# Optimization experiments

Hardware: AMD Instinct MI355X
Metric: run time of the kernel (lower is better)

The kernel has to match this reference:

```python
import jax, jax.numpy as jnp
import numpy as np
from jax import lax

RATE = 2
KSIZE = 3
STRIDE = 1
FUSE_K = 3
SCALE = 10.0
DN = ('NCHW', 'OIHW', 'NCHW')


def extract_patches(x, k, s):
    # x: [B,C,H,W] -> [B,nH,nW,C,k,k]  (ZeroPad2d(1) when k != 1, as in torch code)
    B, C, H, W = x.shape
    p = 0 if k == 1 else 1
    xp = jnp.pad(x, ((0, 0), (0, 0), (p, p), (p, p)))
    nH = (H + 2 * p - k) // s + 1
    nW = (W + 2 * p - k) // s + 1
    cols = [xp[:, :, di:di + s * nH:s, dj:dj + s * nW:s]
            for di in range(k) for dj in range(k)]
    pat = jnp.stack(cols, 0).reshape(k, k, B, C, nH, nW)
    return pat.transpose(2, 4, 5, 3, 0, 1)


def _fuse(y):
    # conv of the [L,L] score image with eye(FUSE_K) kernel, same padding
    # == sum of diagonal shifts of the zero-padded image
    L = y.shape[0]
    p = (FUSE_K - 1) // 2
    A = jnp.pad(y, ((p, p), (p, p)))
    out = A[0:L, 0:L]
    for d in range(1, FUSE_K):
        out = out + A[d:d + L, d:d + L]
    return out


def _per_sample(xi, wi, raw_wi, mmi, h, w):
    # xi: [C,h,w]  wi: [L,C,3,3]  raw_wi: [L,C,4,4]  mmi: [L,1,1]
    L = h * w
    norm = jnp.sqrt(jnp.sum(wi * wi, axis=(1, 2, 3), keepdims=True))
    wi_n = wi / jnp.maximum(norm, 1e-4)
    # cosine-similarity conv: [L,h,w]
    yi = lax.conv_general_dilated(xi[None], wi_n, (1, 1), ((1, 1), (1, 1)),
                                  dimension_numbers=DN)[0]
    # fuse pass 1 on [L(patch), L(spatial)]
    y = _fuse(yi.reshape(L, L))
    # transpose (h_p,w_p,h',w') -> (w_p,h_p,w',h'), fuse pass 2, transpose back
    y = y.reshape(h, w, h, w).transpose(1, 0, 3, 2).reshape(L, L)
    y = _fuse(y)
    y = y.reshape(w, h, w, h).transpose(1, 0, 3, 2).reshape(L, h, w)
    y = y * mmi
    y = jax.nn.softmax(y * SCALE, axis=0)
    y = jnp.maximum(y * mmi, 1e-8)
    # conv_transpose2d(y, raw_wi, stride=2, padding=1) as lhs-dilated conv
    Wf = raw_wi[:, :, ::-1, ::-1].transpose(1, 0, 2, 3)  # [C,L,4,4]
    out = lax.conv_general_dilated(y[None], Wf, (1, 1), ((2, 2), (2, 2)),
                                   lhs_dilation=(2, 2),
                                   dimension_numbers=DN)[0]
    return out / 4.0


def reference(x1, x2, mask):
    B, C, H, W = x1.shape
    kernel = 2 * RATE
    raw_w = extract_patches(x1, kernel, RATE * STRIDE)
    x2s = x2[:, :, ::2, ::2]          # F.interpolate scale=0.5, nearest
    h, w = x2s.shape[2], x2s.shape[3]
    L = h * w
    raw_w = raw_w.reshape(B, L, C, kernel, kernel)
    wpat = extract_patches(x2s, KSIZE, STRIDE).reshape(B, L, C, KSIZE, KSIZE)
    # mask is already [B,1,h,w]: bilinear align_corners resize to (h,w) is identity
    m = extract_patches(mask, KSIZE, STRIDE).reshape(B, L, -1).mean(axis=2)
    mm = (m == 0.0).astype(x1.dtype)[:, :, None, None]  # [B,L,1,1]
    f = lambda xi, wi, rwi, mmi: _per_sample(xi, wi, rwi, mmi, h, w)
    return jax.vmap(f)(x2s, wpat, raw_w, mm)  # [B,C,H,W]


def setup_inputs() -> dict:
    key = jax.random.key(0)
    k1, k2 = jax.random.split(key)
    x1 = jax.random.normal(k1, (2, 128, 96, 96), dtype=jnp.float32)
    x2 = jax.random.normal(k2, (2, 128, 96, 96), dtype=jnp.float32)
    mask = jnp.zeros((2, 1, 48, 48), dtype=jnp.float32)
    return {"x1": x1, "x2": x2, "mask": mask}
```

## Files before the change

kernel.cpp:

```cpp
#include <hip/hip_runtime.h>
#include <hip/hip_bf16.h>

#define Cc   128
#define Hh   96
#define hs   48
#define Ls   2304
#define CK   2048
#define KG   384

typedef __attribute__((ext_vector_type(8))) short short8;
typedef __attribute__((ext_vector_type(4))) float f32x4;

__device__ __forceinline__ unsigned short f2bf(float x) {
    unsigned int u = __float_as_uint(x);
    unsigned int r = (u + 0x7fff + ((u >> 16) & 1)) >> 16;
    return (unsigned short)r;
}
__device__ __forceinline__ float bf2f(unsigned short h) {
    return __uint_as_float((unsigned)h << 16);
}

__device__ __forceinline__ f32x4 ld4u(const float* p) {
    f32x4 v; __builtin_memcpy(&v, p, 16); return v;
}

#define GLOAD_LDS16(g, l) \
    __builtin_amdgcn_global_load_lds((__attribute__((address_space(1))) const void*)(g), \
                                     (__attribute__((address_space(3))) void*)(l), 16, 0, 0)


__global__ __launch_bounds__(256) void transposePQ_k(const float* __restrict__ x2,
                                                     unsigned short* __restrict__ P,
                                                     unsigned short* __restrict__ Q,
                                                     long long sPQ, int z0) {
    const int z = z0 + blockIdx.z;
    const float* x2b = x2 + (size_t)z * Cc * Hh * Hh;
    unsigned short* Pb = P + (size_t)blockIdx.z * sPQ;
    unsigned short* Qb = Q + (size_t)blockIdx.z * sPQ;
    __shared__ float tile[64][65];
    const int c0 = blockIdx.x * 64;
    const int l0 = blockIdx.y * 64;
    const int t = threadIdx.x;
    const int lt = t & 63, cg = t >> 6;
    const int l = l0 + lt;
    const int iy = l / hs, jx = l % hs;
    const int srcoff = iy * (2 * Hh) + 2 * jx;
#pragma unroll
    for (int cc = 0; cc < 16; ++cc) {
        int c = cg * 16 + cc;
        tile[lt][c] = x2b[(size_t)(c0 + c) * (Hh * Hh) + srcoff];
    }
    __syncthreads();
    const int lr = t >> 2, seg = t & 3;
    const int lw = l0 + lr;
    short8 hv0, hv1, lv0, lv1;
#pragma unroll
    for (int k = 0; k < 8; ++k) {
        float x = tile[lr][seg * 16 + k];
        unsigned short h = f2bf(x);
        float hf = __uint_as_float((unsigned)h << 16);
        unsigned short lo = f2bf(x - hf);
        hv0[k] = (short)h; lv0[k] = (short)lo;
    }
#pragma unroll
    for (int k = 0; k < 8; ++k) {
        float x = tile[lr][seg * 16 + 8 + k];
        unsigned short h = f2bf(x);
        float hf = __uint_as_float((unsigned)h << 16);
        unsigned short lo = f2bf(x - hf);
        hv1[k] = (short)h; lv1[k] = (short)lo;
    }
    size_t rowp = (size_t)lw * KG;
    int coff = c0 + seg * 16;
    *(short8*)&Pb[rowp + coff] = hv0;        *(short8*)&Pb[rowp + coff + 8] = hv1;
    *(short8*)&Pb[rowp + 128 + coff] = lv0;  *(short8*)&Pb[rowp + 128 + coff + 8] = lv1;
    *(short8*)&Pb[rowp + 256 + coff] = hv0;  *(short8*)&Pb[rowp + 256 + coff + 8] = hv1;
    *(short8*)&Qb[rowp + coff] = hv0;        *(short8*)&Qb[rowp + coff + 8] = hv1;
    *(short8*)&Qb[rowp + 128 + coff] = hv0;  *(short8*)&Qb[rowp + 128 + coff + 8] = hv1;
    *(short8*)&Qb[rowp + 256 + coff] = lv0;  *(short8*)&Qb[rowp + 256 + coff + 8] = lv1;
}

__global__ __launch_bounds__(256) void mm_k(const float* __restrict__ mask, float* __restrict__ MM) {
    int z = blockIdx.y;
    const float* mb = mask + (size_t)z * hs * hs;
    float* MMb = MM + (size_t)z * Ls;
    int l = blockIdx.x * 256 + threadIdx.x;
    if (l >= Ls) return;
    int ly = l / hs, lx = l % hs;
    float s = 0.f;
    for (int dy = -1; dy <= 1; ++dy)
        for (int dx = -1; dx <= 1; ++dx) {
            int yy = ly + dy, xx = lx + dx;
            if ((unsigned)yy < (unsigned)hs && (unsigned)xx < (unsigned)hs) s += mb[yy * hs + xx];
        }
    float m = s * (1.0f / 9.0f);
    MMb[l] = (m == 0.0f) ? 1.0f : 0.0f;
}

__global__ __launch_bounds__(256) void taps9rn_k(const float* __restrict__ G, float* __restrict__ S,
                                                 float* __restrict__ RN, long long zsG, long long zsS, int z0) {
    const float* Gb = G + (size_t)blockIdx.z * zsG;
    float* Sb = S + (size_t)blockIdx.z * zsS;
    float* RNb = RN + (size_t)(z0 + blockIdx.z) * Ls;
    int g = blockIdx.x * 256 + threadIdx.x;
    int i = g / 576;
    int jb = (g - i * 576) * 4;
    int iy = i / hs, ix = i % hs;
    int jy = jb / hs, jx0 = jb % hs;
    f32x4 acc = {};
#pragma unroll
    for (int dy = -1; dy <= 1; ++dy) {
        int vy = ((unsigned)(iy + dy) < (unsigned)hs) && ((unsigned)(jy + dy) < (unsigned)hs);
#pragma unroll
        for (int dx = -1; dx <= 1; ++dx) {
            int vi = vy && ((unsigned)(ix + dx) < (unsigned)hs);
            int o = hs * dy + dx;
            int row = vi ? (i + o) : i;
            f32x4 v = ld4u(&Gb[(size_t)row * Ls + jb + o]);
            f32x4 m;
#pragma unroll
            for (int ln = 0; ln < 4; ++ln)
                m[ln] = (vi && ((unsigned)(jx0 + ln + dx) < (unsigned)hs)) ? 1.f : 0.f;
            acc += v * m;
        }
    }
    __builtin_memcpy(&Sb[(size_t)i * Ls + jb], &acc, 16);
    int dd = i - jb;
    if ((unsigned)dd < 4u) RNb[i] = 1.0f / fmaxf(sqrtf(acc[dd]), 1e-4f);
}

__global__ __launch_bounds__(256) void fuse12T_k(const float* __restrict__ S, const float* __restrict__ RN,
                                                 float* __restrict__ ZT, long long zsS, long long zsZT, int z0) {
    const float* Sb = S + (size_t)blockIdx.z * zsS;
    float* ZTb = ZT + (size_t)blockIdx.z * zsZT;
    const float* RNb = RN + (size_t)(z0 + blockIdx.z) * Ls;
    __shared__ float tile[64][65];
    const int i0 = blockIdx.y * 64, j0 = blockIdx.x * 64;
    const int t = threadIdx.x;
    const int jg = t & 15, tit = t >> 4;
    const int jb = j0 + jg * 4;
    const int jy0 = jb / hs, jx0 = jb % hs;

    int ccb[9]; f32x4 m4[9];
#pragma unroll
    for (int d2 = -1; d2 <= 1; ++d2) {
        int cl[4], vb[4];
#pragma unroll
        for (int ln = 0; ln < 4; ++ln) {
            int j2 = (jx0 + ln) * hs + jy0 + d2;
            int vv = ((unsigned)j2 < (unsigned)Ls) ? 1 : 0;
            int c = vv ? ((j2 % hs) * hs + j2 / hs) : 0;
            cl[ln] = c; vb[ln] = vv;
        }
        int base = 0;
#pragma unroll
        for (int ln = 0; ln < 4; ++ln) if (vb[ln]) base = cl[ln] - ln;
#pragma unroll
        for (int d1 = -1; d1 <= 1; ++d1) {
            int idx = (d2 + 1) * 3 + (d1 + 1);
            ccb[idx] = base + d1;
            f32x4 mm;
#pragma unroll
            for (int ln = 0; ln < 4; ++ln) {
                int cc = cl[ln] + d1;
                mm[ln] = (vb[ln] && ((unsigned)cc < (unsigned)Ls)) ? 1.f : 0.f;
            }
            m4[idx] = mm;
        }
    }

    f32x4 acc[4] = {};
#pragma unroll
    for (int kk = 0; kk < 4; ++kk) {
        const int i = i0 + tit * 4 + kk;
        const int iy = i / hs, ix = i % hs;
        const int tif = ix * hs + iy;
#pragma unroll
        for (int d2 = -1; d2 <= 1; ++d2) {
            int i2 = tif + d2;
            int vi = ((unsigned)i2 < (unsigned)Ls) ? 1 : 0;
            int r = vi ? ((i2 % hs) * hs + i2 / hs) : 1;
#pragma unroll
            for (int d1 = -1; d1 <= 1; ++d1) {
                int rr = r + d1;
                int vr = vi && ((unsigned)rr < (unsigned)Ls);
                int rrc = vr ? rr : 0;
                float w = RNb[rrc];
                w = vr ? w : 0.f;
                int idx = (d2 + 1) * 3 + (d1 + 1);
                f32x4 v = ld4u(&Sb[(size_t)rrc * Ls + ccb[idx]]);
                acc[kk] += v * m4[idx] * w;
            }
        }
    }
#pragma unroll
    for (int kk = 0; kk < 4; ++kk) {
        int ti = tit * 4 + kk;
        tile[ti][jg * 4 + 0] = acc[kk][0];
        tile[ti][jg * 4 + 1] = acc[kk][1];
        tile[ti][jg * 4 + 2] = acc[kk][2];
        tile[ti][jg * 4 + 3] = acc[kk][3];
    }
    __syncthreads();
    const int r2 = t >> 2, cs = (t & 3) * 16;
    float vbuf[16];
#pragma unroll
    for (int k = 0; k < 16; ++k) vbuf[k] = tile[cs + k][r2];
    float* dst = &ZTb[(size_t)(j0 + r2) * Ls + i0 + cs];
#pragma unroll
    for (int k = 0; k < 4; ++k)
        *(float4*)&dst[k * 4] = *(float4*)&vbuf[k * 4];
}

__global__ __launch_bounds__(256) void softmax_row_k(const float* __restrict__ ZT, const float* __restrict__ MM,
                                                     unsigned short* __restrict__ AT, long long zsZT, int z0) {
    const int z = z0 + blockIdx.z;
    const float* ZTb = ZT + (size_t)blockIdx.z * zsZT;
    const float* MMb = MM + (size_t)z * Ls;
    unsigned short* ATb = AT + (size_t)z * Ls * Ls;
    const int w = threadIdx.x >> 6, lane = threadIdx.x & 63;
    const int p = blockIdx.x * 4 + w;
    const float* row = ZTb + (size_t)p * Ls;
    float v[36];
    float mx = -3.4e38f;
#pragma unroll
    for (int k = 0; k < 9; ++k) {
        const float4 zv = *(const float4*)&row[k * 256 + lane * 4];
        const float4 m = *(const float4*)&MMb[k * 256 + lane * 4];
        v[4 * k + 0] = zv.x * m.x * 10.f;
        v[4 * k + 1] = zv.y * m.y * 10.f;
        v[4 * k + 2] = zv.z * m.z * 10.f;
        v[4 * k + 3] = zv.w * m.w * 10.f;
        mx = fmaxf(mx, fmaxf(fmaxf(v[4 * k], v[4 * k + 1]), fmaxf(v[4 * k + 2], v[4 * k + 3])));
    }
#pragma unroll
    for (int off = 32; off; off >>= 1) mx = fmaxf(mx, __shfl_xor(mx, off));
    float sum = 0.f;
#pragma unroll
    for (int kk = 0; kk < 36; ++kk) { v[kk] = expf(v[kk] - mx); sum += v[kk]; }
#pragma unroll
    for (int off = 32; off; off >>= 1) sum += __shfl_xor(sum, off);
    const float rs = 1.0f / sum;
#pragma unroll
    for (int k = 0; k < 9; ++k) {
        const float4 m = *(const float4*)&MMb[k * 256 + lane * 4];
        ushort4 o;
        o.x = f2bf(fmaxf(v[4 * k + 0] * rs * m.x, 1e-8f));
        o.y = f2bf(fmaxf(v[4 * k + 1] * rs * m.y, 1e-8f));
        o.z = f2bf(fmaxf(v[4 * k + 2] * rs * m.z, 1e-8f));
        o.w = f2bf(fmaxf(v[4 * k + 3] * rs * m.w, 1e-8f));
        *(ushort4*)&ATb[(size_t)p * Ls + k * 256 + lane * 4] = o;
    }
}

__global__ __launch_bounds__(256) void gather_rwT_k(const float* __restrict__ x1, unsigned short* __restrict__ RWT) {
    const int z = blockIdx.z;
    const float* x1b = x1 + (size_t)z * Cc * Hh * Hh;
    unsigned short* R = RWT + (size_t)z * CK * Ls;
    int l = blockIdx.x * 256 + threadIdx.x;
    int ck = blockIdx.y;
    int c = ck >> 4, a = (ck >> 2) & 3, b2 = ck & 3;
    int ly = l / hs, lx = l % hs;
    int u = 2 * ly + a - 1, vv = 2 * lx + b2 - 1;
    float val = ((unsigned)u < (unsigned)Hh && (unsigned)vv < (unsigned)Hh) ? x1b[c * (Hh * Hh) + u * Hh + vv] : 0.0f;
    R[(size_t)ck * Ls + l] = f2bf(val);
}

__global__ __launch_bounds__(256) void scatter3_k(const unsigned short* __restrict__ T, float* __restrict__ out) {
    const int z = blockIdx.z;
    const int c = blockIdx.x;
    const int yh = blockIdx.y;
    const unsigned short* Tb = T + (size_t)z * Ls * CK + (size_t)c * 16;
    float* outb = out + (size_t)z * Cc * Hh * Hh + (size_t)c * Hh * Hh;
    const int i0 = (yh == 0) ? 0 : 23;
    __shared__ unsigned short Tl[1200 * 16];
    const int t = threadIdx.x;
#pragma unroll
    for (int rep = 0; rep < 5; ++rep) {
        int p = rep * 256 + t;
        if (p < 1200)
            __builtin_memcpy(&Tl[p * 16], &Tb[(size_t)(i0 * hs + p) * CK], 32);
    }
    __syncthreads();
#pragma unroll
    for (int rep = 0; rep < 5; ++rep) {
        int idx4 = rep * 256 + t;
        if (idx4 >= 1152) break;
        int Y = yh * 48 + idx4 / 24;
        int X0 = (idx4 % 24) * 4;
        float o4[4];
#pragma unroll
        for (int xi = 0; xi < 4; ++xi) {
            int X = X0 + xi;
            int a0 = (Y + 1) & 1, b0 = (X + 1) & 1;
            float s = 0.f;
#pragma unroll
            for (int ai = 0; ai < 2; ++ai) {
                int a = a0 + 2 * ai;
                int i = (Y + 1 - a) >> 1;
                if ((unsigned)i >= (unsigned)hs) continue;
#pragma unroll
                for (int bi = 0; bi < 2; ++bi) {
                    int b2 = b0 + 2 * bi;
                    int jj = (X + 1 - b2) >> 1;
                    if ((unsigned)jj >= (unsigned)hs) continue;
                    s += bf2f(Tl[((i - i0) * hs + jj) * 16 + a * 4 + b2]);
                }
            }
            o4[xi] = 0.25f * s;
        }
        *(float4*)&outb[Y * Hh + X0] = *(float4*)&o4[0];
    }
}

template <int SUPER, int CBF16>
__global__ __launch_bounds__(256) void mfma_gemm_k(const unsigned short* __restrict__ A,
                                                   const unsigned short* __restrict__ Bt,
                                                   void* __restrict__ Cv, int M, int N, int K,
                                                   long long sA, long long sB, long long sC) {
    A  += (size_t)blockIdx.z * sA;
    Bt += (size_t)blockIdx.z * sB;
    float* Cf = (float*)Cv + (CBF16 ? 0 : (size_t)blockIdx.z * sC);
    unsigned short* Ch = (unsigned short*)Cv + (CBF16 ? (size_t)blockIdx.z * sC : 0);

    const int nb = gridDim.x * gridDim.y;
    const int flat = blockIdx.y * gridDim.x + blockIdx.x;
    const int q = nb >> 3, r = nb & 7;
    const int xcd = flat & 7, sidx = flat >> 3;
    const int wg = (xcd < r ? xcd * (q + 1) : r * (q + 1) + (xcd - r) * q) + sidx;
    int bm, bn;
    if (SUPER) {
        int st = wg / 12, tt = wg % 12;
        int stn = st & 3, stm = st >> 2;
        int tn = tt & 3, tm = tt >> 2;
        bn = (stn * 4 + tn) * 128;
        bm = (stm * 3 + tm) * 128;
    } else {
        bm = (wg / gridDim.x) * 128;
        bn = (wg % gridDim.x) * 128;
    }

    __shared__ __align__(16) unsigned short Asm[2][128 * 32];
    __shared__ __align__(16) unsigned short Bsm[2][128 * 32];
    const int t = threadIdx.x;
    const int lane = t & 63, w = t >> 6;
    const int wr = w >> 1, wc = w & 1;

    const int rA = 32 * w + (lane >> 2);
    const int kA = (((lane & 3) ^ ((lane >> 3) & 3))) * 8;
    const unsigned short* gA0 = A + (size_t)(bm + rA) * K + kA;
    const unsigned short* gA1 = gA0 + (size_t)16 * K;
    const unsigned short* gB0 = Bt + (size_t)(bn + rA) * K + kA;
    const unsigned short* gB1 = gB0 + (size_t)16 * K;

#define STAGE4(b, koff) do { \
        GLOAD_LDS16(gA0 + (koff), &Asm[b][(2 * w) * 512]); \
        GLOAD_LDS16(gA1 + (koff), &Asm[b][(2 * w + 1) * 512]); \
        GLOAD_LDS16(gB0 + (koff), &Bsm[b][(2 * w) * 512]); \
        GLOAD_LDS16(gB1 + (koff), &Bsm[b][(2 * w + 1) * 512]); \
    } while (0)

    const int fr = lane & 15, fq = lane >> 4;
    const int sxa = (fr >> 1) & 3;
    const int sqa = (fq ^ sxa) * 8;
    f32x4 acc[4][4] = {};

    const int nt = K >> 5;
    STAGE4(0, 0);
    __syncthreads();
    int cur = 0;
    for (int tt = 0; tt < nt; ++tt) {
        if (tt + 1 < nt) STAGE4(cur ^ 1, (tt + 1) * 32);
        short8 av[4], bv[4];
#pragma unroll
        for (int m = 0; m < 4; ++m)
            av[m] = *(const short8*)&Asm[cur][(wr * 64 + m * 16 + fr) * 32 + sqa];
#pragma unroll
        for (int n = 0; n < 4; ++n)
            bv[n] = *(const short8*)&Bsm[cur][(wc * 64 + n * 16 + fr) * 32 + sqa];
#pragma unroll
        for (int m = 0; m < 4; ++m)
#pragma unroll
            for (int n = 0; n < 4; ++n)
                acc[m][n] = __builtin_amdgcn_mfma_f32_16x16x32_bf16(av[m], bv[n], acc[m][n], 0, 0, 0);
        __syncthreads();
        cur ^= 1;
    }
#undef STAGE4

#pragma unroll
    for (int m = 0; m < 4; ++m) {
        int row0 = bm + wr * 64 + m * 16 + fq * 4;
#pragma unroll
        for (int n = 0; n < 4; ++n) {
            int col = bn + wc * 64 + n * 16 + fr;
#pragma unroll
            for (int rr = 0; rr < 4; ++rr) {
                if (CBF16)
                    Ch[(size_t)(row0 + rr) * N + col] = f2bf(acc[m][n][rr]);
                else
                    Cf[(size_t)(row0 + rr) * N + col] = acc[m][n][rr];
            }
        }
    }
}


extern "C" void kernel_launch(void* const* d_in, const int* in_sizes, int n_in,
                              void* d_out, int out_size, void* d_ws, size_t ws_size,
                              hipStream_t stream) {
    const float* x1 = (const float*)d_in[0];
    const float* x2 = (const float*)d_in[1];
    const float* mask = (const float*)d_in[2];
    float* out = (float*)d_out;

    char* base = (char*)d_ws;
    const size_t LsLs = (size_t)Ls * Ls;
    const size_t LsCK = (size_t)Ls * CK;
    const long long sPQ = (long long)Ls * KG;

    const bool batched = ws_size >= 132175872ull;

    float* MM2 = (float*)(base);
    float* RN2 = (float*)(base + 20480);
    unsigned short *P, *Q, *ATb2, *RWT2;
    float *G, *S;
    unsigned short* T2 = (unsigned short*)base;
    if (batched) {
        P    = (unsigned short*)(base + 40960);
        Q    = (unsigned short*)(base + 3584000);
        G    = (float*)(base + 7127040);
        S    = (float*)(base + 49598464);
        ATb2 = (unsigned short*)(base + 92067840);
        RWT2 = (unsigned short*)(base + 113301504);
    } else {
        P    = (unsigned short*)(base + 40960);
        Q    = (unsigned short*)(base + 1812480);
        G    = (float*)(base + 3586048);
        S    = (float*)(base + 24823808);
        ATb2 = (unsigned short*)(base + 46059520);
        RWT2 = (unsigned short*)(base + 67293184);
    }

    mm_k<<<dim3(Ls / 256, 2), 256, 0, stream>>>(mask, MM2);
    gather_rwT_k<<<dim3(Ls / 256, CK, 2), 256, 0, stream>>>(x1, RWT2);

    const int tapsGrid = (Ls * 576) / 256;

    if (batched) {
        transposePQ_k<<<dim3(2, Ls / 64, 2), 256, 0, stream>>>(x2, P, Q, sPQ, 0);
        mfma_gemm_k<0, 0><<<dim3(Ls / 128, Ls / 128, 2), 256, 0, stream>>>(
            P, Q, G, Ls, Ls, KG, sPQ, sPQ, (long long)LsLs);
        taps9rn_k<<<dim3(tapsGrid, 1, 2), 256, 0, stream>>>(G, S, RN2, (long long)LsLs, (long long)LsLs, 0);
        fuse12T_k<<<dim3(Ls / 64, Ls / 64, 2), 256, 0, stream>>>(S, RN2, G, (long long)LsLs, (long long)LsLs, 0);
        softmax_row_k<<<dim3(Ls / 4, 1, 2), 256, 0, stream>>>(G, MM2, ATb2, (long long)LsLs, 0);
    } else {
        for (int z0 = 0; z0 < 2; ++z0) {
            transposePQ_k<<<dim3(2, Ls / 64, 1), 256, 0, stream>>>(x2, P, Q, 0, z0);
            mfma_gemm_k<0, 0><<<dim3(Ls / 128, Ls / 128, 1), 256, 0, stream>>>(
                P, Q, G, Ls, Ls, KG, 0, 0, 0);
            taps9rn_k<<<dim3(tapsGrid, 1, 1), 256, 0, stream>>>(G, S, RN2, 0, 0, z0);
            fuse12T_k<<<dim3(Ls / 64, Ls / 64, 1), 256, 0, stream>>>(S, RN2, G, 0, 0, z0);
            softmax_row_k<<<dim3(Ls / 4, 1, 1), 256, 0, stream>>>(G, MM2, ATb2, 0, z0);
        }
    }

    mfma_gemm_k<1, 1><<<dim3(CK / 128, Ls / 128, 2), 256, 0, stream>>>(
        ATb2, RWT2, T2, Ls, CK, Ls,
        (long long)LsLs, (long long)LsCK, (long long)LsCK);

    scatter3_k<<<dim3(Cc, 2, 2), 256, 0, stream>>>(T2, out);

    (void)in_sizes; (void)n_in; (void)out_size; (void)ws_size;
}
```

Measured before the change: 222.1 us.

## Triple-buffer GEMM LDS pipeline, vectorize patch gather, use fast exp

The bf16 MFMA GEMM goes from double to triple LDS buffering. It prefetches two k-tiles ahead and replaces __syncthreads with an explicit vmcnt wait plus s_barrier, so global loads overlap more with compute. The raw-patch gather kernel now has each thread write 8 bf16 values as a single 16-byte store, with a flattened 1D grid, which cuts index math and store transactions. Softmax uses __expf in place of expf, trading slight accuracy for cheaper exponentials. The manual vmcnt accounting depends on the exact number of loads issued per stage and risks races if that assumption breaks.

```diff
diff --git a/kernel.cpp b/kernel.cpp
--- a/kernel.cpp
+++ b/kernel.cpp
@@ -237,7 +237,7 @@
     for (int off = 32; off; off >>= 1) mx = fmaxf(mx, __shfl_xor(mx, off));
     float sum = 0.f;
 #pragma unroll
-    for (int kk = 0; kk < 36; ++kk) { v[kk] = expf(v[kk] - mx); sum += v[kk]; }
+    for (int kk = 0; kk < 36; ++kk) { v[kk] = __expf(v[kk] - mx); sum += v[kk]; }
 #pragma unroll
     for (int off = 32; off; off >>= 1) sum += __shfl_xor(sum, off);
     const float rs = 1.0f / sum;
@@ -257,13 +257,24 @@
     const int z = blockIdx.z;
     const float* x1b = x1 + (size_t)z * Cc * Hh * Hh;
     unsigned short* R = RWT + (size_t)z * CK * Ls;
-    int l = blockIdx.x * 256 + threadIdx.x;
-    int ck = blockIdx.y;
+    int idx = blockIdx.x * 256 + threadIdx.x;
+    int ck = idx / 288;
+    int lg = idx - ck * 288;
+    int l0 = lg * 8;
+    int ly = lg / 6;
+    int lx0 = (lg - ly * 6) * 8;
     int c = ck >> 4, a = (ck >> 2) & 3, b2 = ck & 3;
-    int ly = l / hs, lx = l % hs;
-    int u = 2 * ly + a - 1, vv = 2 * lx + b2 - 1;
-    float val = ((unsigned)u < (unsigned)Hh && (unsigned)vv < (unsigned)Hh) ? x1b[c * (Hh * Hh) + u * Hh + vv] : 0.0f;
-    R[(size_t)ck * Ls + l] = f2bf(val);
+    int u = 2 * ly + a - 1;
+    short8 o = {};
+    if ((unsigned)u < (unsigned)Hh) {
+        const float* row = x1b + (size_t)c * (Hh * Hh) + (size_t)u * Hh;
+#pragma unroll
+        for (int e = 0; e < 8; ++e) {
+            int vv = 2 * (lx0 + e) + b2 - 1;
+            o[e] = (short)(((unsigned)vv < (unsigned)Hh) ? f2bf(row[vv]) : (unsigned short)0);
+        }
+    }
+    *(short8*)&R[(size_t)ck * Ls + l0] = o;
 }
 
 __global__ __launch_bounds__(256) void scatter3_k(const unsigned short* __restrict__ T, float* __restrict__ out) {
@@ -340,8 +351,8 @@
         bn = (wg % gridDim.x) * 128;
     }
 
-    __shared__ __align__(16) unsigned short Asm[2][128 * 32];
-    __shared__ __align__(16) unsigned short Bsm[2][128 * 32];
+    __shared__ __align__(16) unsigned short Asm[3][128 * 32];
+    __shared__ __align__(16) unsigned short Bsm[3][128 * 32];
     const int t = threadIdx.x;
     const int lane = t & 63, w = t >> 6;
     const int wr = w >> 1, wc = w & 1;
@@ -361,16 +372,19 @@
     } while (0)
 
     const int fr = lane & 15, fq = lane >> 4;
-    const int sxa = (fr >> 1) & 3;
-    const int sqa = (fq ^ sxa) * 8;
+    const int sqa = (fq ^ ((fr >> 1) & 3)) * 8;
     f32x4 acc[4][4] = {};
 
     const int nt = K >> 5;
     STAGE4(0, 0);
-    __syncthreads();
+    STAGE4(1, 32);
+    asm volatile("s_waitcnt vmcnt(4)" ::: "memory");
+    __builtin_amdgcn_s_barrier();
+    __builtin_amdgcn_sched_barrier(0);
+
     int cur = 0;
     for (int tt = 0; tt < nt; ++tt) {
-        if (tt + 1 < nt) STAGE4(cur ^ 1, (tt + 1) * 32);
+        if (tt + 2 < nt) STAGE4((tt + 2) % 3, (tt + 2) * 32);
         short8 av[4], bv[4];
 #pragma unroll
         for (int m = 0; m < 4; ++m)
@@ -383,8 +397,16 @@
 #pragma unroll
             for (int n = 0; n < 4; ++n)
                 acc[m][n] = __builtin_amdgcn_mfma_f32_16x16x32_bf16(av[m], bv[n], acc[m][n], 0, 0, 0);
-        __syncthreads();
-        cur ^= 1;
+        __builtin_amdgcn_sched_barrier(0);
+        if (tt + 1 < nt) {
+            if (tt + 2 < nt)
+                asm volatile("s_waitcnt vmcnt(4)" ::: "memory");
+            else
+                asm volatile("s_waitcnt vmcnt(0)" ::: "memory");
+            __builtin_amdgcn_s_barrier();
+            __builtin_amdgcn_sched_barrier(0);
+        }
+        cur = (cur + 1) % 3;
     }
 #undef STAGE4
 
@@ -443,7 +465,7 @@
     }
 
     mm_k<<<dim3(Ls / 256, 2), 256, 0, stream>>>(mask, MM2);
-    gather_rwT_k<<<dim3(Ls / 256, CK, 2), 256, 0, stream>>>(x1, RWT2);
+    gather_rwT_k<<<dim3((CK * 288) / 256, 1, 2), 256, 0, stream>>>(x1, RWT2);
 
     const int tapsGrid = (Ls * 576) / 256;
 
```

Result: slower. 237.7 us (+7.0%).
